# Kernel optimization log

Hardware: AMD Instinct MI355X
Metric: run time of the kernel (lower is better)

The kernel has to match this reference:

```python
import jax, jax.numpy as jnp
import numpy as np

N = 50000   # nodes
E = 800000  # edges (avg degree 16)
F = 128     # node_features


def setup_inputs() -> dict:
    key = jax.random.key(0)
    ks = jax.random.split(key, 10)
    s = 1.0 / np.sqrt(F)
    x = jax.random.normal(ks[0], (N, F), jnp.float32)
    edge_index = jax.random.randint(ks[1], (2, E), 0, N, dtype=jnp.int32)
    edge_weight = jax.random.uniform(ks[2], (E,), jnp.float32)
    # EvolveGCNO initial weight (glorot-ish) and GRU parameters (PyTorch layout)
    W0 = jax.random.uniform(ks[3], (F, F), jnp.float32, -s, s)
    W_ih = jax.random.uniform(ks[4], (3 * F, F), jnp.float32, -s, s)
    W_hh = jax.random.uniform(ks[5], (3 * F, F), jnp.float32, -s, s)
    b_ih = jax.random.uniform(ks[6], (3 * F,), jnp.float32, -s, s)
    b_hh = jax.random.uniform(ks[7], (3 * F,), jnp.float32, -s, s)
    # Linear(F, 1) head
    w_lin = jax.random.uniform(ks[8], (1, F), jnp.float32, -s, s)
    b_lin = jax.random.uniform(ks[9], (1,), jnp.float32, -s, s)
    return dict(x=x, edge_index=edge_index, edge_weight=edge_weight, W0=W0,
                W_ih=W_ih, W_hh=W_hh, b_ih=b_ih, b_hh=b_hh,
                w_lin=w_lin, b_lin=b_lin)


def _gru_evolve(W0, W_ih, W_hh, b_ih, b_hh):
    # GRU(input=W0, hidden=W0): seq_len=1, batch=F, feature=F (PyTorch gate order r,z,n)
    gi = W0 @ W_ih.T + b_ih  # [F, 3F]
    gh = W0 @ W_hh.T + b_hh  # [F, 3F]
    f = W0.shape[1]
    i_r, i_z, i_n = gi[:, :f], gi[:, f:2 * f], gi[:, 2 * f:]
    h_r, h_z, h_n = gh[:, :f], gh[:, f:2 * f], gh[:, 2 * f:]
    r = jax.nn.sigmoid(i_r + h_r)
    z = jax.nn.sigmoid(i_z + h_z)
    n = jnp.tanh(i_n + r * h_n)
    return (1.0 - z) * n + z * W0  # evolved weight [F, F]


def reference(x, edge_index, edge_weight, W0, W_ih, W_hh, b_ih, b_hh, w_lin, b_lin):
    n_nodes = x.shape[0]
    W = _gru_evolve(W0, W_ih, W_hh, b_ih, b_hh)
    # gcn_norm: add self loops (weight 1), symmetric D^-1/2 A D^-1/2
    loop = jnp.arange(n_nodes, dtype=edge_index.dtype)
    src = jnp.concatenate([edge_index[0], loop])
    dst = jnp.concatenate([edge_index[1], loop])
    w = jnp.concatenate([edge_weight, jnp.ones((n_nodes,), x.dtype)])
    deg = jax.ops.segment_sum(w, dst, num_segments=n_nodes)
    dinv = jnp.where(deg > 0, jax.lax.rsqrt(deg), 0.0)
    norm = dinv[src] * w * dinv[dst]  # [E+N]
    xw = x @ W  # [N, F]
    h = jax.ops.segment_sum(norm[:, None] * xw[src], dst, num_segments=n_nodes)
    h = jnp.tanh(h)
    return h @ w_lin.T + b_lin  # [N, 1]
```

## Files before the change

kernel.cpp:

```cpp
#include <hip/hip_runtime.h>
#include <hip/hip_bf16.h>
#include <hip/hip_fp16.h>
#include <math.h>

#define N_NODES 50000
#define N_EDGES 800000
#define FDIM 128
#define HIST_BLOCKS 3125
#define XW_BLOCKS 391
#define SCAN_BLOCKS 196

typedef unsigned int uint32;
typedef __attribute__((ext_vector_type(8))) __bf16 bf16x8;
typedef __attribute__((ext_vector_type(8))) short short8;
typedef __attribute__((ext_vector_type(16))) float f32x16;

#define FLAG_A 0
#define FLAG_B 1
#define SUMS 8
#define SCANNED 208

__device__ inline unsigned short f2bf(float f) {
  unsigned int u = __float_as_uint(f);
  unsigned int r = u + 0x7fffu + ((u >> 16) & 1u);
  return (unsigned short)(r >> 16);
}

__global__ __launch_bounds__(256) void evolve_kernel(
    const float* __restrict__ W0, const float* __restrict__ Wih,
    const float* __restrict__ Whh, const float* __restrict__ bih,
    const float* __restrict__ bhh, unsigned short* __restrict__ Wb,
    int* __restrict__ cnt, int* __restrict__ sync) {
  int bid = blockIdx.x;
  int t = threadIdx.x;
  int gid = bid * 256 + t;
  for (int j = gid; j < N_NODES; j += 128 * 256) cnt[j] = 0;
  if (gid < 8) sync[gid] = 0;

  __shared__ float w0s[FDIM];
  __shared__ float gis[3 * FDIM];
  __shared__ float ghs[3 * FDIM];
  if (t < FDIM) w0s[t] = W0[bid * FDIM + t];
  __syncthreads();
  for (int jj = t; jj < 3 * FDIM; jj += 256) {
    float gi = bih[jj], gh = bhh[jj];
    const float4* wih4 = (const float4*)(Wih + jj * FDIM);
    const float4* whh4 = (const float4*)(Whh + jj * FDIM);
#pragma unroll 8
    for (int k = 0; k < FDIM / 4; k++) {
      float4 a = wih4[k];
      float4 b = whh4[k];
      float w0a = w0s[4 * k], w0b = w0s[4 * k + 1];
      float w0c = w0s[4 * k + 2], w0d = w0s[4 * k + 3];
      gi += a.x * w0a + a.y * w0b + a.z * w0c + a.w * w0d;
      gh += b.x * w0a + b.y * w0b + b.z * w0c + b.w * w0d;
    }
    gis[jj] = gi;
    ghs[jj] = gh;
  }
  __syncthreads();
  if (t < FDIM) {
    float r = 1.0f / (1.0f + expf(-(gis[t] + ghs[t])));
    float z = 1.0f / (1.0f + expf(-(gis[t + FDIM] + ghs[t + FDIM])));
    float nn = tanhf(gis[t + 2 * FDIM] + r * ghs[t + 2 * FDIM]);
    float w = (1.0f - z) * nn + z * w0s[t];
    Wb[((((bid >> 3) << 7) | t) << 3) | (bid & 7)] = f2bf(w);
  }
}

__global__ void histxw_kernel(const int* __restrict__ ei,
                              int* __restrict__ cnt, int* __restrict__ rank,
                              const float* __restrict__ x,
                              const unsigned short* __restrict__ Wb,
                              unsigned short* __restrict__ y, int n) {
  int t = threadIdx.x;
  int bid = blockIdx.x;
  if (bid < HIST_BLOCKS) {
    int idx = bid * 256 + t;
    int dst = ei[N_EDGES + idx];
    rank[idx] = atomicAdd(&cnt[dst], 1);
    return;
  }
  int lane = t & 63;
  int wid = (bid - HIST_BLOCKS) * 4 + (t >> 6);
  int tr = wid * 32;
  if (tr >= n) return;
  int m = lane & 31;
  int q2 = lane >> 5;

  int row = tr + m;
  if (row >= n) row = n - 1;
  const float* xr = x + (size_t)row * FDIM;

  bf16x8 a[8];
#pragma unroll
  for (int kc = 0; kc < 8; kc++) {
    int k0 = kc * 16 + q2 * 8;
    float4 p = *(const float4*)(xr + k0);
    float4 q = *(const float4*)(xr + k0 + 4);
    short8 s;
    s[0] = (short)f2bf(p.x); s[1] = (short)f2bf(p.y);
    s[2] = (short)f2bf(p.z); s[3] = (short)f2bf(p.w);
    s[4] = (short)f2bf(q.x); s[5] = (short)f2bf(q.y);
    s[6] = (short)f2bf(q.z); s[7] = (short)f2bf(q.w);
    a[kc] = __builtin_bit_cast(bf16x8, s);
  }

  f32x16 acc[4];
#pragma unroll
  for (int ct = 0; ct < 4; ct++) {
#pragma unroll
    for (int r = 0; r < 16; r++) acc[ct][r] = 0.0f;
  }
#pragma unroll
  for (int ct = 0; ct < 4; ct++) {
    int nn = ct * 32 + m;
#pragma unroll
    for (int kc = 0; kc < 8; kc++) {
      int kg = kc * 2 + q2;
      bf16x8 b = __builtin_bit_cast(
          bf16x8, *(const short8*)(Wb + (((kg << 7) + nn) << 3)));
      acc[ct] = __builtin_amdgcn_mfma_f32_32x32x16_bf16(a[kc], b, acc[ct], 0,
                                                        0, 0);
    }
  }

#pragma unroll
  for (int r = 0; r < 16; r++) {
    int rl = (r & 3) + ((r >> 2) << 3) + (q2 << 2);
    int rg = tr + rl;
    if (rg < n) {
#pragma unroll
      for (int ct = 0; ct < 4; ct++) {
        y[(size_t)rg * FDIM + ct * 32 + m] = f2bf(acc[ct][r]);
      }
    }
  }
}

__global__ __launch_bounds__(256) void scan_all_kernel(
    const int* __restrict__ cnt, int* __restrict__ sync, int* __restrict__ offs,
    int n) {
  __shared__ int tmp[256];
  int t = threadIdx.x;
  int bid = blockIdx.x;
  int idx = bid * 256 + t;
  int v = (idx < n) ? cnt[idx] : 0;
  tmp[t] = v;
  __syncthreads();
#pragma unroll
  for (int off = 1; off < 256; off <<= 1) {
    int u = (t >= off) ? tmp[t - off] : 0;
    __syncthreads();
    tmp[t] += u;
    __syncthreads();
  }
  int local_excl = tmp[t] - v;
  int block_sum = tmp[255];
  if (t == 0) {
    __hip_atomic_store(&sync[SUMS + bid], block_sum, __ATOMIC_RELEASE,
                       __HIP_MEMORY_SCOPE_AGENT);
    __hip_atomic_fetch_add(&sync[FLAG_A], 1, __ATOMIC_ACQ_REL,
                           __HIP_MEMORY_SCOPE_AGENT);
  }
  if (bid == 0) {
    if (t == 0) {
      while (__hip_atomic_load(&sync[FLAG_A], __ATOMIC_ACQUIRE,
                               __HIP_MEMORY_SCOPE_AGENT) < SCAN_BLOCKS) {
        __builtin_amdgcn_s_sleep(1);
      }
    }
    __syncthreads();
    __shared__ int ps[256];
    int pv = (t < SCAN_BLOCKS)
                 ? __hip_atomic_load(&sync[SUMS + t], __ATOMIC_RELAXED,
                                     __HIP_MEMORY_SCOPE_AGENT)
                 : 0;
    ps[t] = pv;
    __syncthreads();
#pragma unroll
    for (int off = 1; off < 256; off <<= 1) {
      int u = (t >= off) ? ps[t - off] : 0;
      __syncthreads();
      ps[t] += u;
      __syncthreads();
    }
    if (t < SCAN_BLOCKS)
      __hip_atomic_store(&sync[SCANNED + t], ps[t] - pv, __ATOMIC_RELAXED,
                         __HIP_MEMORY_SCOPE_AGENT);
    __syncthreads();
    if (t == 0)
      __hip_atomic_store(&sync[FLAG_B], 1, __ATOMIC_RELEASE,
                         __HIP_MEMORY_SCOPE_AGENT);
  }
  if (t == 0) {
    while (__hip_atomic_load(&sync[FLAG_B], __ATOMIC_ACQUIRE,
                             __HIP_MEMORY_SCOPE_AGENT) == 0) {
      __builtin_amdgcn_s_sleep(1);
    }
  }
  __syncthreads();
  int base = __hip_atomic_load(&sync[SCANNED + bid], __ATOMIC_RELAXED,
                               __HIP_MEMORY_SCOPE_AGENT);
  int excl = base + local_excl;
  if (idx < n) offs[idx] = excl;
  if (idx == n - 1) offs[n] = excl + v;
}

__global__ void scatter_kernel(const int* __restrict__ ei,
                               const float* __restrict__ ew,
                               const int* __restrict__ offs,
                               const int* __restrict__ rank,
                               uint32* __restrict__ csr, int e) {
  int idx = blockIdx.x * blockDim.x + threadIdx.x;
  if (idx < e) {
    int src = ei[idx];
    int dst = ei[N_EDGES + idx];
    unsigned short h = __half_as_ushort(__float2half(ew[idx]));
    csr[offs[dst] + rank[idx]] = ((uint32)h << 16) | (uint32)src;
  }
}

__global__ __launch_bounds__(256) void deg_dinv_kernel(
    const uint32* __restrict__ csr, const int* __restrict__ offs,
    float* __restrict__ dinv, int n) {
  int i = blockIdx.x * blockDim.x + threadIdx.x;
  if (i >= n) return;
  int b = offs[i], e = offs[i + 1];
  float d = 1.0f;
  for (int j = b; j < e; j++)
    d += __half2float(__ushort_as_half((unsigned short)(csr[j] >> 16)));
  dinv[i] = rsqrtf(d);
}

__global__ __launch_bounds__(256) void gather_kernel(
    const uint32* __restrict__ yb, const int* __restrict__ offs,
    const uint32* __restrict__ csr, const float* __restrict__ dinv,
    const float* __restrict__ wl, const float* __restrict__ bl,
    float* __restrict__ out, int n) {
  int wid = (int)((blockIdx.x * (size_t)blockDim.x + threadIdx.x) >> 6);
  int lane = threadIdx.x & 63;
  if (wid >= n) return;
  float di = dinv[wid];
  uint32 uv = yb[(size_t)wid * 64 + lane];
  float ax = di * __uint_as_float(uv << 16);
  float ay = di * __uint_as_float(uv & 0xffff0000u);
  int beg = offs[wid], end = offs[wid + 1];
  int e = beg;
  for (; e + 8 <= end; e += 8) {
    uint32 c[8];
    uint32 u[8];
    float dv[8];
#pragma unroll
    for (int q = 0; q < 8; q++) c[q] = csr[e + q];
#pragma unroll
    for (int q = 0; q < 8; q++) u[q] = yb[(size_t)(c[q] & 0xffffu) * 64 + lane];
#pragma unroll
    for (int q = 0; q < 8; q++) dv[q] = dinv[c[q] & 0xffffu];
#pragma unroll
    for (int q = 0; q < 8; q++) {
      float wn =
          __half2float(__ushort_as_half((unsigned short)(c[q] >> 16))) * dv[q];
      ax += wn * __uint_as_float(u[q] << 16);
      ay += wn * __uint_as_float(u[q] & 0xffff0000u);
    }
  }
  for (; e < end; e++) {
    uint32 c = csr[e];
    uint32 u = yb[(size_t)(c & 0xffffu) * 64 + lane];
    float wn = __half2float(__ushort_as_half((unsigned short)(c >> 16))) *
               dinv[c & 0xffffu];
    ax += wn * __uint_as_float(u << 16);
    ay += wn * __uint_as_float(u & 0xffff0000u);
  }
  float2 wv = ((const float2*)wl)[lane];
  float p = tanhf(di * ax) * wv.x + tanhf(di * ay) * wv.y;
#pragma unroll
  for (int o = 32; o > 0; o >>= 1) p += __shfl_down(p, o, 64);
  if (lane == 0) out[wid] = p + bl[0];
}

extern "C" void kernel_launch(void* const* d_in, const int* in_sizes, int n_in,
                              void* d_out, int out_size, void* d_ws,
                              size_t ws_size, hipStream_t stream) {
  const float* x = (const float*)d_in[0];
  const int* ei = (const int*)d_in[1];
  const float* ew = (const float*)d_in[2];
  const float* W0 = (const float*)d_in[3];
  const float* Wih = (const float*)d_in[4];
  const float* Whh = (const float*)d_in[5];
  const float* bih = (const float*)d_in[6];
  const float* bhh = (const float*)d_in[7];
  const float* wl = (const float*)d_in[8];
  const float* bl = (const float*)d_in[9];
  float* out = (float*)d_out;

  unsigned short* Wb = (unsigned short*)d_ws;
  unsigned short* y = Wb + 16384;
  float* dinv = (float*)(y + (size_t)N_NODES * FDIM);
  int* cnt = (int*)(dinv + N_NODES);
  int* sync = cnt + N_NODES;
  int* rank = sync + 512;
  int* offs = rank + N_EDGES;
  uint32* csr = (uint32*)(offs + 50008);

  evolve_kernel<<<FDIM, 256, 0, stream>>>(W0, Wih, Whh, bih, bhh, Wb, cnt,
                                          sync);
  histxw_kernel<<<HIST_BLOCKS + XW_BLOCKS, 256, 0, stream>>>(ei, cnt, rank, x,
                                                             Wb, y, N_NODES);
  scan_all_kernel<<<SCAN_BLOCKS, 256, 0, stream>>>(cnt, sync, offs, N_NODES);
  scatter_kernel<<<HIST_BLOCKS, 256, 0, stream>>>(ei, ew, offs, rank, csr,
                                                  N_EDGES);
  deg_dinv_kernel<<<SCAN_BLOCKS, 256, 0, stream>>>(csr, offs, dinv, N_NODES);
  gather_kernel<<<(N_NODES * 64) / 256, 256, 0, stream>>>(
      (const uint32*)y, offs, csr, dinv, wl, bl, out, N_NODES);
}
```

Baseline: 220.9 us.

## Pack degree sum into 64-bit histogram atomics and prenormalize CSR edge weights

The histogram pass now does one 64-bit atomic per edge, carrying the count in the high word and the fixed-point edge weight in the low word, with four edges handled per thread. The scan computes dinv directly from that packed value, so the separate degree kernel is dropped. The scatter stores the fully normalized weight (w*dinv[src]*dinv[dst]) in fp16, which removes the per-edge dinv gather from the hot gather loop. The cost is fixed-point rounding of the degree sum and extra fp16 precision loss on the normalized weights.

```diff
diff --git a/kernel.cpp b/kernel.cpp
--- a/kernel.cpp
+++ b/kernel.cpp
@@ -6,11 +6,15 @@
 #define N_NODES 50000
 #define N_EDGES 800000
 #define FDIM 128
-#define HIST_BLOCKS 3125
+#define HIST_BLOCKS 782
+#define HIST_STRIDE (HIST_BLOCKS * 256)
 #define XW_BLOCKS 391
 #define SCAN_BLOCKS 196
+#define FIX_SCALE 1048576.0f
+#define FIX_INV (1.0f / 1048576.0f)
 
 typedef unsigned int uint32;
+typedef unsigned long long uint64;
 typedef __attribute__((ext_vector_type(8))) __bf16 bf16x8;
 typedef __attribute__((ext_vector_type(8))) short short8;
 typedef __attribute__((ext_vector_type(16))) float f32x16;
@@ -30,11 +34,11 @@
     const float* __restrict__ W0, const float* __restrict__ Wih,
     const float* __restrict__ Whh, const float* __restrict__ bih,
     const float* __restrict__ bhh, unsigned short* __restrict__ Wb,
-    int* __restrict__ cnt, int* __restrict__ sync) {
+    int* __restrict__ cnt64i, int* __restrict__ sync) {
   int bid = blockIdx.x;
   int t = threadIdx.x;
   int gid = bid * 256 + t;
-  for (int j = gid; j < N_NODES; j += 128 * 256) cnt[j] = 0;
+  for (int j = gid; j < 2 * N_NODES; j += 128 * 256) cnt64i[j] = 0;
   if (gid < 8) sync[gid] = 0;
 
   __shared__ float w0s[FDIM];
@@ -69,16 +73,38 @@
 }
 
 __global__ void histxw_kernel(const int* __restrict__ ei,
-                              int* __restrict__ cnt, int* __restrict__ rank,
+                              const float* __restrict__ ew,
+                              uint64* __restrict__ cnt64,
+                              int* __restrict__ rank,
                               const float* __restrict__ x,
                               const unsigned short* __restrict__ Wb,
                               unsigned short* __restrict__ y, int n) {
   int t = threadIdx.x;
   int bid = blockIdx.x;
   if (bid < HIST_BLOCKS) {
-    int idx = bid * 256 + t;
-    int dst = ei[N_EDGES + idx];
-    rank[idx] = atomicAdd(&cnt[dst], 1);
+    int gid = bid * 256 + t;
+    int j0 = gid, j1 = gid + HIST_STRIDE, j2 = gid + 2 * HIST_STRIDE,
+        j3 = gid + 3 * HIST_STRIDE;
+    int d0 = ei[N_EDGES + j0];
+    float w0 = ew[j0];
+    int d1 = (j1 < N_EDGES) ? ei[N_EDGES + j1] : 0;
+    float w1 = (j1 < N_EDGES) ? ew[j1] : 0.0f;
+    int d2 = (j2 < N_EDGES) ? ei[N_EDGES + j2] : 0;
+    float w2 = (j2 < N_EDGES) ? ew[j2] : 0.0f;
+    int d3 = (j3 < N_EDGES) ? ei[N_EDGES + j3] : 0;
+    float w3 = (j3 < N_EDGES) ? ew[j3] : 0.0f;
+    uint64 i0 = (1ull << 32) | (uint64)__float2uint_rn(w0 * FIX_SCALE);
+    uint64 i1 = (1ull << 32) | (uint64)__float2uint_rn(w1 * FIX_SCALE);
+    uint64 i2 = (1ull << 32) | (uint64)__float2uint_rn(w2 * FIX_SCALE);
+    uint64 i3 = (1ull << 32) | (uint64)__float2uint_rn(w3 * FIX_SCALE);
+    uint64 r0 = atomicAdd(&cnt64[d0], i0);
+    uint64 r1 = (j1 < N_EDGES) ? atomicAdd(&cnt64[d1], i1) : 0;
+    uint64 r2 = (j2 < N_EDGES) ? atomicAdd(&cnt64[d2], i2) : 0;
+    uint64 r3 = (j3 < N_EDGES) ? atomicAdd(&cnt64[d3], i3) : 0;
+    rank[j0] = (int)(r0 >> 32);
+    if (j1 < N_EDGES) rank[j1] = (int)(r1 >> 32);
+    if (j2 < N_EDGES) rank[j2] = (int)(r2 >> 32);
+    if (j3 < N_EDGES) rank[j3] = (int)(r3 >> 32);
     return;
   }
   int lane = t & 63;
@@ -138,14 +164,17 @@
   }
 }
 
-__global__ __launch_bounds__(256) void scan_all_kernel(
-    const int* __restrict__ cnt, int* __restrict__ sync, int* __restrict__ offs,
-    int n) {
+__global__ __launch_bounds__(256) void scan_dinv_kernel(
+    const uint64* __restrict__ cnt64, int* __restrict__ sync,
+    int* __restrict__ offs, float* __restrict__ dinv, int n) {
   __shared__ int tmp[256];
   int t = threadIdx.x;
   int bid = blockIdx.x;
   int idx = bid * 256 + t;
-  int v = (idx < n) ? cnt[idx] : 0;
+  uint64 cv = (idx < n) ? cnt64[idx] : 0ull;
+  int v = (int)(cv >> 32);
+  if (idx < n)
+    dinv[idx] = rsqrtf(1.0f + (float)(uint32)(cv & 0xffffffffull) * FIX_INV);
   tmp[t] = v;
   __syncthreads();
 #pragma unroll
@@ -211,26 +240,16 @@
                                const float* __restrict__ ew,
                                const int* __restrict__ offs,
                                const int* __restrict__ rank,
+                               const float* __restrict__ dinv,
                                uint32* __restrict__ csr, int e) {
   int idx = blockIdx.x * blockDim.x + threadIdx.x;
   if (idx < e) {
     int src = ei[idx];
     int dst = ei[N_EDGES + idx];
-    unsigned short h = __half_as_ushort(__float2half(ew[idx]));
+    float nrm = ew[idx] * dinv[src] * dinv[dst];
+    unsigned short h = __half_as_ushort(__float2half(nrm));
     csr[offs[dst] + rank[idx]] = ((uint32)h << 16) | (uint32)src;
   }
-}
-
-__global__ __launch_bounds__(256) void deg_dinv_kernel(
-    const uint32* __restrict__ csr, const int* __restrict__ offs,
-    float* __restrict__ dinv, int n) {
-  int i = blockIdx.x * blockDim.x + threadIdx.x;
-  if (i >= n) return;
-  int b = offs[i], e = offs[i + 1];
-  float d = 1.0f;
-  for (int j = b; j < e; j++)
-    d += __half2float(__ushort_as_half((unsigned short)(csr[j] >> 16)));
-  dinv[i] = rsqrtf(d);
 }
 
 __global__ __launch_bounds__(256) void gather_kernel(
@@ -242,25 +261,22 @@
   int lane = threadIdx.x & 63;
   if (wid >= n) return;
   float di = dinv[wid];
+  float sn = di * di;
   uint32 uv = yb[(size_t)wid * 64 + lane];
-  float ax = di * __uint_as_float(uv << 16);
-  float ay = di * __uint_as_float(uv & 0xffff0000u);
+  float ax = sn * __uint_as_float(uv << 16);
+  float ay = sn * __uint_as_float(uv & 0xffff0000u);
   int beg = offs[wid], end = offs[wid + 1];
   int e = beg;
   for (; e + 8 <= end; e += 8) {
     uint32 c[8];
     uint32 u[8];
-    float dv[8];
 #pragma unroll
     for (int q = 0; q < 8; q++) c[q] = csr[e + q];
 #pragma unroll
     for (int q = 0; q < 8; q++) u[q] = yb[(size_t)(c[q] & 0xffffu) * 64 + lane];
 #pragma unroll
-    for (int q = 0; q < 8; q++) dv[q] = dinv[c[q] & 0xffffu];
-#pragma unroll
     for (int q = 0; q < 8; q++) {
-      float wn =
-          __half2float(__ushort_as_half((unsigned short)(c[q] >> 16))) * dv[q];
+      float wn = __half2float(__ushort_as_half((unsigned short)(c[q] >> 16)));
       ax += wn * __uint_as_float(u[q] << 16);
       ay += wn * __uint_as_float(u[q] & 0xffff0000u);
     }
@@ -268,13 +284,12 @@
   for (; e < end; e++) {
     uint32 c = csr[e];
     uint32 u = yb[(size_t)(c & 0xffffu) * 64 + lane];
-    float wn = __half2float(__ushort_as_half((unsigned short)(c >> 16))) *
-               dinv[c & 0xffffu];
+    float wn = __half2float(__ushort_as_half((unsigned short)(c >> 16)));
     ax += wn * __uint_as_float(u << 16);
     ay += wn * __uint_as_float(u & 0xffff0000u);
   }
   float2 wv = ((const float2*)wl)[lane];
-  float p = tanhf(di * ax) * wv.x + tanhf(di * ay) * wv.y;
+  float p = tanhf(ax) * wv.x + tanhf(ay) * wv.y;
 #pragma unroll
   for (int o = 32; o > 0; o >>= 1) p += __shfl_down(p, o, 64);
   if (lane == 0) out[wid] = p + bl[0];
@@ -298,20 +313,20 @@
   unsigned short* Wb = (unsigned short*)d_ws;
   unsigned short* y = Wb + 16384;
   float* dinv = (float*)(y + (size_t)N_NODES * FDIM);
-  int* cnt = (int*)(dinv + N_NODES);
-  int* sync = cnt + N_NODES;
+  uint64* cnt64 = (uint64*)(dinv + N_NODES);
+  int* sync = (int*)(cnt64 + N_NODES);
   int* rank = sync + 512;
   int* offs = rank + N_EDGES;
   uint32* csr = (uint32*)(offs + 50008);
 
-  evolve_kernel<<<FDIM, 256, 0, stream>>>(W0, Wih, Whh, bih, bhh, Wb, cnt,
-                                          sync);
-  histxw_kernel<<<HIST_BLOCKS + XW_BLOCKS, 256, 0, stream>>>(ei, cnt, rank, x,
-                                                             Wb, y, N_NODES);
-  scan_all_kernel<<<SCAN_BLOCKS, 256, 0, stream>>>(cnt, sync, offs, N_NODES);
-  scatter_kernel<<<HIST_BLOCKS, 256, 0, stream>>>(ei, ew, offs, rank, csr,
-                                                  N_EDGES);
-  deg_dinv_kernel<<<SCAN_BLOCKS, 256, 0, stream>>>(csr, offs, dinv, N_NODES);
+  evolve_kernel<<<FDIM, 256, 0, stream>>>(W0, Wih, Whh, bih, bhh, Wb,
+                                          (int*)cnt64, sync);
+  histxw_kernel<<<HIST_BLOCKS + XW_BLOCKS, 256, 0, stream>>>(
+      ei, ew, cnt64, rank, x, Wb, y, N_NODES);
+  scan_dinv_kernel<<<SCAN_BLOCKS, 256, 0, stream>>>(cnt64, sync, offs, dinv,
+                                                    N_NODES);
+  scatter_kernel<<<(N_EDGES + 255) / 256, 256, 0, stream>>>(ei, ew, offs, rank,
+                                                            dinv, csr, N_EDGES);
   gather_kernel<<<(N_NODES * 64) / 256, 256, 0, stream>>>(
       (const uint32*)y, offs, csr, dinv, wl, bl, out, N_NODES);
 }
```

Measured after the change: 219.5 us. No clear change (-0.6%).
